# Performance work log

Measured on AMD Instinct MI355X. Metric: run time of the kernel, lower is better.

The kernel has to match this reference:

```python
import jax, jax.numpy as jnp
import numpy as np

S = 3072        # total packed tokens
E = 1280        # d_model
H = 20          # encoder_attention_heads
D = E // H      # head_dim = 64
NSEG = 16       # number of packed audio chunks


def setup_inputs() -> dict:
    key = jax.random.key(0)
    ks = jax.random.split(key, 9)
    w = lambda k, shape: (jax.random.normal(k, shape, jnp.float32) * 0.02)
    hidden_states = jax.random.normal(ks[0], (S, E), jnp.float32)
    cu_seqlens = (jnp.arange(NSEG + 1, dtype=jnp.int32) * (S // NSEG))
    return {
        "hidden_states": hidden_states,
        "Wq": w(ks[1], (E, E)), "bq": w(ks[2], (E,)),
        "Wk": w(ks[3], (E, E)),                      # k_proj has no bias
        "Wv": w(ks[4], (E, E)), "bv": w(ks[5], (E,)),
        "Wo": w(ks[6], (E, E)), "bo": w(ks[7], (E,)),
        "cu_seqlens": cu_seqlens,
    }


def reference(hidden_states, Wq, bq, Wk, Wv, bv, Wo, bo, cu_seqlens):
    Sq, Em = hidden_states.shape
    Dh = Em // H
    # projections (torch Linear: x @ W.T + b)
    q = (hidden_states @ Wq.T + bq).reshape(Sq, H, Dh).transpose(1, 0, 2)  # [H,S,D]
    k = (hidden_states @ Wk.T).reshape(Sq, H, Dh).transpose(1, 0, 2)       # [H,S,D]
    v = (hidden_states @ Wv.T + bv).reshape(Sq, H, Dh).transpose(1, 0, 2)  # [H,S,D]
    # block-diagonal additive mask from cu_seqlens (vectorized equivalent of
    # the original Python loop): tokens attend only within their own segment.
    pos = jnp.arange(Sq)
    seg = jnp.searchsorted(cu_seqlens[1:], pos, side="right")              # segment id per token
    same = seg[:, None] == seg[None, :]                                    # [S,S]
    bias = jnp.where(same, 0.0, jnp.finfo(q.dtype).min)
    attn = jnp.einsum("hqd,hkd->hqk", q, k) / np.sqrt(Dh).astype(q.dtype)  # [H,S,S]
    attn = jax.nn.softmax(attn + bias, axis=-1)
    out = jnp.einsum("hqk,hkd->hqd", attn, v)                              # [H,S,D]
    out = out.transpose(1, 0, 2).reshape(Sq, Em)
    return out @ Wo.T + bo
```

## Files before the change

kernel.cpp:

```cpp
#include <hip/hip_runtime.h>
#include <hip/hip_bf16.h>
#include <stdint.h>

#define S_TOK 3072
#define E_DIM 1280
#define H_NUM 20
#define D_HEAD 64
#define NSEG 16

typedef __attribute__((ext_vector_type(8))) short short8;
typedef __attribute__((ext_vector_type(4))) float f32x4;

__device__ __forceinline__ unsigned short f2bf(float f){
  union { float f; unsigned int i; } u; u.f = f;
  unsigned int r = u.i + 0x7FFFu + ((u.i >> 16) & 1u);
  return (unsigned short)(r >> 16);
}

__device__ __forceinline__ void gload_lds16(const void* g, void* l){
  __builtin_amdgcn_global_load_lds((__attribute__((address_space(1))) void*)(g),
                                   (__attribute__((address_space(3))) void*)(l), 16, 0, 0);
}

__global__ void cvt_all(const float* __restrict__ hs,
                        const float* __restrict__ w0, const float* __restrict__ w1,
                        const float* __restrict__ w2,
                        unsigned short* __restrict__ hsb,
                        unsigned short* __restrict__ dqkv,
                        int nHS4, int nW4){
  int i = blockIdx.x * blockDim.x + threadIdx.x;
  const float* src;
  unsigned short* dst;
  size_t sj, dj;
  if (i < nHS4){
    src = hs; dst = hsb; sj = i; dj = i;
  } else {
    int t = i - nHS4;
    int w = t / nW4;
    if (w >= 3) return;
    int j = t - w * nW4;
    src = (w == 0) ? w0 : (w == 1) ? w1 : w2;
    sj = j;
    dst = dqkv; dj = (size_t)w * nW4 + j;
  }
  float4 v = reinterpret_cast<const float4*>(src)[sj];
  ushort4 o;
  o.x = f2bf(v.x); o.y = f2bf(v.y); o.z = f2bf(v.z); o.w = f2bf(v.w);
  reinterpret_cast<ushort4*>(dst)[dj] = o;
}

template<int MODE>
__global__ __launch_bounds__(MODE==0?512:256, MODE==0?2:2) void gemm_ph(
    const unsigned short* __restrict__ A,
    const unsigned short* __restrict__ Bp,
    const float* __restrict__ bias0,
    const float* __restrict__ bias1,
    unsigned short* __restrict__ Oq,
    unsigned short* __restrict__ Ok,
    unsigned short* __restrict__ Ov,
    float* __restrict__ Of,
    int M, int N, int K)
{
  constexpr int BM    = MODE==0 ? 256 : 128;
  constexpr int BLOCK = MODE==0 ? 512 : 256;
  constexpr int HR    = BM/2;
  constexpr int HS    = HR*64;
  constexpr int MR2   = MODE==0 ? 4 : 2;

  __shared__ __align__(16) unsigned short SH[8*HS];

  const int nwg = gridDim.x;
  const int xcd = blockIdx.x & 7, ix = blockIdx.x >> 3;
  const int qq = nwg >> 3, rr8 = nwg & 7;
  const int wg = (xcd < rr8 ? xcd*(qq+1) : rr8*(qq+1) + (xcd-rr8)*qq) + ix;
  const int nbn = N / BM;
  const int sgn = nbn / 5;
  const int st = wg / 20, ii = wg % 20;
  const int bm = (st / sgn) * 4 + ii / 5;
  const int bn = (st % sgn) * 5 + ii % 5;
  const int row0 = bm * BM, col0 = bn * BM;

  const int tid  = threadIdx.x;
  const int lane = tid & 63;
  const int w    = tid >> 6;
  const int wm   = MODE==0 ? (w >> 2) : (w >> 1);
  const int wn   = MODE==0 ? (w & 3) : (w & 1);

  const f32x4 fz = {0.f, 0.f, 0.f, 0.f};
  f32x4 acc[4][MR2][2];
#pragma unroll
  for (int qd = 0; qd < 4; ++qd)
#pragma unroll
    for (int m = 0; m < MR2; ++m)
#pragma unroll
      for (int n = 0; n < 2; ++n) acc[qd][m][n] = fz;

  const int s1 = tid, s2 = BLOCK + tid;
  const int r1 = s1 >> 3, ks1 = (s1 & 7) ^ (r1 & 7);
  const int r2 = s2 >> 3, ks2 = (s2 & 7) ^ (r2 & 7);

  auto stA = [&](int h, int t){
    unsigned short* d = SH + ((t & 1) * 4 + h) * HS;
    const unsigned short* g = A + (size_t)(row0 + h*HR) * K + (t << 6);
    gload_lds16(g + (size_t)r1*K + ks1*8, d + s1*8);
    gload_lds16(g + (size_t)r2*K + ks2*8, d + s2*8);
  };
  auto stB = [&](int h, int t){
    unsigned short* d = SH + ((t & 1) * 4 + 2 + h) * HS;
    const unsigned short* g = Bp + (size_t)(col0 + h*HR) * K + (t << 6);
    gload_lds16(g + (size_t)r1*K + ks1*8, d + s1*8);
    gload_lds16(g + (size_t)r2*K + ks2*8, d + s2*8);
  };

  short8 af[MR2][2], bf0[2][2], bf1[2][2];
  auto RA = [&](int mh, int db){
    const unsigned short* Ah = SH + (db*4 + mh)*HS;
#pragma unroll
    for (int m = 0; m < MR2; ++m){
      int ra = wm*(HR/2) + m*16 + (lane & 15);
#pragma unroll
      for (int kk = 0; kk < 2; ++kk){
        int sl = kk*4 + (lane >> 4);
        af[m][kk] = *reinterpret_cast<const short8*>(&Ah[ra*64 + ((sl ^ (ra & 7)))*8]);
      }
    }
  };
  auto RB = [&](int nh, int db, short8 (*bf)[2]){
    const unsigned short* Bh = SH + (db*4 + 2 + nh)*HS;
#pragma unroll
    for (int n = 0; n < 2; ++n){
      int rb = wn*32 + n*16 + (lane & 15);
#pragma unroll
      for (int kk = 0; kk < 2; ++kk){
        int sl = kk*4 + (lane >> 4);
        bf[n][kk] = *reinterpret_cast<const short8*>(&Bh[rb*64 + ((sl ^ (rb & 7)))*8]);
      }
    }
  };

#define MF_Q(QD, BF)                                                          \
  do {                                                                        \
    __builtin_amdgcn_s_setprio(1);                                            \
    _Pragma("unroll")                                                         \
    for (int kk = 0; kk < 2; ++kk)                                            \
      _Pragma("unroll")                                                       \
      for (int m = 0; m < MR2; ++m)                                           \
        _Pragma("unroll")                                                     \
        for (int n = 0; n < 2; ++n)                                           \
          acc[QD][m][n] = __builtin_amdgcn_mfma_f32_16x16x32_bf16(            \
              af[m][kk], BF[n][kk], acc[QD][m][n], 0, 0, 0);                  \
    __builtin_amdgcn_s_setprio(0);                                            \
  } while (0)

#define LGKM0 do { asm volatile("s_waitcnt lgkmcnt(0)" ::: "memory");         \
                   __builtin_amdgcn_sched_barrier(0); } while (0)
#define BAR   __builtin_amdgcn_s_barrier()

  const int nk = K >> 6;
  stA(0,0); stB(0,0); stB(1,0); stA(1,0);
  stA(0,1); stB(0,1); stB(1,1);
  asm volatile("s_waitcnt vmcnt(6)" ::: "memory");
  BAR;

  for (int t = 0; t < nk - 1; ++t){
    const int db = t & 1;
    const bool f2 = (t + 2 < nk);
    RA(0, db); RB(0, db, bf0);
    stA(1, t+1);
    BAR; LGKM0; MF_Q(0, bf0); BAR;
    RB(1, db, bf1);
    if (f2) stA(0, t+2);
    BAR; LGKM0; MF_Q(1, bf1); BAR;
    RA(1, db);
    if (f2) stB(0, t+2);
    BAR; LGKM0; MF_Q(2, bf1); BAR;
    if (f2) stB(1, t+2);
    BAR; MF_Q(3, bf0);
    if (f2) asm volatile("s_waitcnt vmcnt(6)" ::: "memory");
    else    asm volatile("s_waitcnt vmcnt(4)" ::: "memory");
    BAR;
  }
  {
    const int db = (nk - 1) & 1;
    RA(0, db); RB(0, db, bf0);
    BAR; LGKM0; MF_Q(0, bf0);
    asm volatile("s_waitcnt vmcnt(2)" ::: "memory");
    BAR;
    RB(1, db, bf1);
    BAR; LGKM0; MF_Q(1, bf1);
    asm volatile("s_waitcnt vmcnt(0)" ::: "memory");
    BAR;
    RA(1, db);
    BAR; LGKM0; MF_Q(2, bf1); BAR;
    MF_Q(3, bf0);
  }
  __syncthreads();

  if (MODE == 0){
    unsigned short* Cs = SH;
    const int CSTR = 264;
    const int mat = col0 / E_DIM;
    const int cc0 = col0 - mat * E_DIM;
    unsigned short* dst = (mat == 0) ? Oq : ((mat == 1) ? Ok : Ov);
    float bb[2][2];
#pragma unroll
    for (int nh = 0; nh < 2; ++nh)
#pragma unroll
      for (int n = 0; n < 2; ++n){
        int cc = cc0 + nh*128 + wn*32 + n*16 + (lane & 15);
        bb[nh][n] = (mat == 0) ? bias0[cc] : (mat == 2 ? bias1[cc] : 0.0f);
      }
#pragma unroll
    for (int ph = 0; ph < 2; ++ph){
#pragma unroll
      for (int q2i = 0; q2i < 2; ++q2i){
        const int qd = ph*2 + q2i;
        const int nh = (qd >> 1) ^ (qd & 1);
#pragma unroll
        for (int m = 0; m < MR2; ++m)
#pragma unroll
          for (int n = 0; n < 2; ++n)
#pragma unroll
            for (int j = 0; j < 4; ++j){
              int rr = wm*64 + m*16 + (lane >> 4)*4 + j;
              int c  = nh*128 + wn*32 + n*16 + (lane & 15);
              Cs[rr * CSTR + c] = f2bf(acc[qd][m][n][j] + bb[nh][n]);
            }
      }
      __syncthreads();
#pragma unroll
      for (int i = 0; i < 8; ++i){
        int tk  = i * 512 + tid;
        int p   = tk >> 10;
        int idx = tk & 1023;
        int rr  = idx >> 3, sq = idx & 7;
        short8 vv = *reinterpret_cast<const short8*>(&Cs[rr * CSTR + p * 64 + sq * 8]);
        int gr = row0 + ph * 128 + rr;
        int hh = (cc0 >> 6) + p;
        *reinterpret_cast<short8*>(&dst[((size_t)hh * S_TOK + gr) * D_HEAD + sq * 8]) = vv;
      }
      __syncthreads();
    }
  } else {
    float bc[2][2];
#pragma unroll
    for (int nh = 0; nh < 2; ++nh)
#pragma unroll
      for (int n = 0; n < 2; ++n)
        bc[nh][n] = bias0[col0 + nh*64 + wn*32 + n*16 + (lane & 15)];
#pragma unroll
    for (int qd = 0; qd < 4; ++qd){
      const int mh = qd >> 1;
      const int nh = (qd >> 1) ^ (qd & 1);
#pragma unroll
      for (int m = 0; m < MR2; ++m)
#pragma unroll
        for (int n = 0; n < 2; ++n){
          int c = col0 + nh*64 + wn*32 + n*16 + (lane & 15);
#pragma unroll
          for (int j = 0; j < 4; ++j){
            int r = row0 + mh*64 + wm*32 + m*16 + (lane >> 4)*4 + j;
            Of[(size_t)r * E_DIM + c] = acc[qd][m][n][j] + bc[nh][n];
          }
        }
    }
  }
#undef MF_Q
#undef LGKM0
#undef BAR
}

#define VSTR 200
#define PSTR 72
#define ATTN_BLKS (H_NUM * NSEG * 3)
__global__ __launch_bounds__(256, 3) void attn_kernel(
    const unsigned short* __restrict__ Q,
    const unsigned short* __restrict__ Kb,
    const unsigned short* __restrict__ V,
    const int* __restrict__ cu,
    unsigned short* __restrict__ O,
    const float* __restrict__ Wo,
    unsigned short* __restrict__ wob,
    int nW4)
{
  __shared__ __align__(16) unsigned short Vt[64*VSTR];
  __shared__ __align__(16) unsigned short Pw[4][16][PSTR];

  const int bid  = blockIdx.x;
  if (bid >= ATTN_BLKS){
    int i = (bid - ATTN_BLKS) * 256 + threadIdx.x;
    if (i < nW4){
      float4 v = reinterpret_cast<const float4*>(Wo)[i];
      ushort4 o;
      o.x = f2bf(v.x); o.y = f2bf(v.y); o.z = f2bf(v.z); o.w = f2bf(v.w);
      reinterpret_cast<ushort4*>(wob)[i] = o;
    }
    return;
  }
  const int unit = bid / 3;
  const int third= bid - unit*3;
  const int h    = unit >> 4;
  const int seg  = unit & 15;
  const int s0   = cu[seg];
  const int L    = cu[seg + 1] - s0;
  if (L <= 0) return;

  const int tid  = threadIdx.x;
  const int lane = tid & 63;
  const int w    = tid >> 6;
  const int row0g = third*64 + w*16;

  const unsigned short* qh = Q  + (size_t)h * S_TOK * D_HEAD;
  const unsigned short* kh = Kb + (size_t)h * S_TOK * D_HEAD;
  const unsigned short* vh = V  + (size_t)h * S_TOK * D_HEAD;

#pragma unroll
  for (int i = 0; i < 6; ++i){
    int task = i*256 + tid;
    int sr   = task % 192;
    int grp  = task / 192;
    int svr  = s0 + (sr < L ? sr : L - 1);
    short8 vv = *reinterpret_cast<const short8*>(vh + (size_t)svr*64 + grp*8);
#pragma unroll
    for (int j = 0; j < 8; ++j) Vt[(grp*8 + j)*VSTR + sr] = (unsigned short)vv[j];
  }

  short8 qf[2];
#pragma unroll
  for (int kk = 0; kk < 2; ++kk){
    int r  = row0g + (lane & 15);
    int sr = s0 + (r < L ? r : L - 1);
    qf[kk] = *reinterpret_cast<const short8*>(qh + (size_t)sr*64 + kk*32 + (lane >> 4)*8);
  }

  __syncthreads();

  const f32x4 fz = {0.f, 0.f, 0.f, 0.f};
  const float SCL = 0.125f * 1.44269504088896f;

  f32x4 sacc[12];
#pragma unroll
  for (int nt = 0; nt < 12; ++nt) sacc[nt] = fz;

#pragma unroll
  for (int nt = 0; nt < 12; ++nt){
    int rb = nt*16 + (lane & 15);
    int sr = s0 + (rb < L ? rb : L - 1);
    const unsigned short* kr = kh + (size_t)sr*64 + (lane >> 4)*8;
    short8 kf0 = *reinterpret_cast<const short8*>(kr);
    short8 kf1 = *reinterpret_cast<const short8*>(kr + 32);
    sacc[nt] = __builtin_amdgcn_mfma_f32_16x16x32_bf16(qf[0], kf0, sacc[nt], 0, 0, 0);
    sacc[nt] = __builtin_amdgcn_mfma_f32_16x16x32_bf16(qf[1], kf1, sacc[nt], 0, 0, 0);
  }

  float rinv[4];
#pragma unroll
  for (int j = 0; j < 4; ++j){
    float mx = -1e30f;
#pragma unroll
    for (int nt = 0; nt < 12; ++nt){
      int c = nt*16 + (lane & 15);
      float vv = (c < L) ? sacc[nt][j] : -1e30f;
      sacc[nt][j] = vv;
      mx = fmaxf(mx, vv);
    }
    mx = fmaxf(mx, __shfl_xor(mx, 1, 64));
    mx = fmaxf(mx, __shfl_xor(mx, 2, 64));
    mx = fmaxf(mx, __shfl_xor(mx, 4, 64));
    mx = fmaxf(mx, __shfl_xor(mx, 8, 64));
    float sum = 0.f;
#pragma unroll
    for (int nt = 0; nt < 12; ++nt){
      float pp = exp2f((sacc[nt][j] - mx) * SCL);
      sacc[nt][j] = pp;
      sum += pp;
    }
    sum += __shfl_xor(sum, 1, 64);
    sum += __shfl_xor(sum, 2, 64);
    sum += __shfl_xor(sum, 4, 64);
    sum += __shfl_xor(sum, 8, 64);
    rinv[j] = 1.0f / sum;
  }

  f32x4 oacc[4];
#pragma unroll
  for (int nt = 0; nt < 4; ++nt) oacc[nt] = fz;

#pragma unroll
  for (int kk = 0; kk < 6; ++kk){
#pragma unroll
    for (int ntl = 0; ntl < 2; ++ntl){
      int nt = kk*2 + ntl;
#pragma unroll
      for (int j = 0; j < 4; ++j)
        Pw[w][(lane >> 4)*4 + j][ntl*16 + (lane & 15)] = f2bf(sacc[nt][j]);
    }
    short8 pf = *reinterpret_cast<const short8*>(&Pw[w][lane & 15][(lane >> 4)*8]);
#pragma unroll
    for (int nt4 = 0; nt4 < 4; ++nt4){
      int dcol = nt4*16 + (lane & 15);
      short8 vf = *reinterpret_cast<const short8*>(&Vt[dcol*VSTR + kk*32 + (lane >> 4)*8]);
      oacc[nt4] = __builtin_amdgcn_mfma_f32_16x16x32_bf16(pf, vf, oacc[nt4], 0, 0, 0);
    }
  }

#pragma unroll
  for (int nt4 = 0; nt4 < 4; ++nt4)
#pragma unroll
    for (int j = 0; j < 4; ++j)
      Pw[w][(lane >> 4)*4 + j][nt4*16 + (lane & 15)] = f2bf(oacc[nt4][j] * rinv[j]);

  {
    int r = lane >> 2;
    int gr = row0g + r;
    if (gr < L){
#pragma unroll
      for (int part = 0; part < 2; ++part){
        int c0 = (lane & 3)*16 + part*8;
        short8 vv = *reinterpret_cast<const short8*>(&Pw[w][r][c0]);
        *reinterpret_cast<short8*>(&O[(size_t)(s0 + gr) * E_DIM + h*64 + c0]) = vv;
      }
    }
  }
}

extern "C" void kernel_launch(void* const* d_in, const int* in_sizes, int n_in,
                              void* d_out, int out_size, void* d_ws, size_t ws_size,
                              hipStream_t stream)
{
  const float* hs = (const float*)d_in[0];
  const float* Wq = (const float*)d_in[1];
  const float* bq = (const float*)d_in[2];
  const float* Wk = (const float*)d_in[3];
  const float* Wv = (const float*)d_in[4];
  const float* bv = (const float*)d_in[5];
  const float* Wo = (const float*)d_in[6];
  const float* bo = (const float*)d_in[7];
  const int*   cu = (const int*)d_in[8];
  float* out = (float*)d_out;

  unsigned short* p = (unsigned short*)d_ws;
  unsigned short* hsb  = p; p += (size_t)S_TOK * E_DIM;
  unsigned short* wqkv = p; p += (size_t)3 * E_DIM * E_DIM;
  unsigned short* wob  = p; p += (size_t)E_DIM * E_DIM;
  unsigned short* qb   = p; p += (size_t)S_TOK * E_DIM;
  unsigned short* kb   = p; p += (size_t)S_TOK * E_DIM;
  unsigned short* vb   = p; p += (size_t)S_TOK * E_DIM;
  unsigned short* aob  = p; p += (size_t)S_TOK * E_DIM;

  const int nHS4 = S_TOK * E_DIM / 4;
  const int nW4  = E_DIM * E_DIM / 4;
  const int nCvt = nHS4 + 3 * nW4;
  cvt_all<<<(nCvt + 255) / 256, 256, 0, stream>>>(hs, Wq, Wk, Wv, hsb, wqkv, nHS4, nW4);

  gemm_ph<0><<<(S_TOK/256) * (3*E_DIM/256), 512, 0, stream>>>(
      hsb, wqkv, bq, bv, qb, kb, vb, nullptr, S_TOK, 3*E_DIM, E_DIM);

  const int cvtWoBlks = (nW4 + 255) / 256;
  attn_kernel<<<ATTN_BLKS + cvtWoBlks, 256, 0, stream>>>(
      qb, kb, vb, cu, aob, Wo, wob, nW4);

  gemm_ph<1><<<(S_TOK/128) * (E_DIM/128), 256, 0, stream>>>(
      aob, wob, bo, nullptr, nullptr, nullptr, nullptr, out, S_TOK, E_DIM, E_DIM);
}
```

Baseline: 95.49 us.

## Retile QKV GEMM to 192x256 blocks and shorten prefetch pipeline

The QKV projection GEMM drops its shared template and uses 192x256 tiles, so the grid goes from 180 to 240 workgroups, which fills the CUs of the 256-CU part better. Its double-buffered pipeline now prefetches one k-step ahead with fewer barriers per iteration instead of two steps ahead. The output GEMM becomes its own kernel with the same restructured one-ahead pipeline. The trade-off is a shallower prefetch, which leaves less room to hide global load latency, plus a more complex tile-index mapping and epilogue.

```diff
diff --git a/kernel.cpp b/kernel.cpp
--- a/kernel.cpp
+++ b/kernel.cpp
@@ -49,8 +49,11 @@
   reinterpret_cast<ushort4*>(dst)[dj] = o;
 }
 
-template<int MODE>
-__global__ __launch_bounds__(MODE==0?512:256, MODE==0?2:2) void gemm_ph(
+#define LGKM0 do { asm volatile("s_waitcnt lgkmcnt(0)" ::: "memory");         \
+                   __builtin_amdgcn_sched_barrier(0); } while (0)
+#define BAR   __builtin_amdgcn_s_barrier()
+
+__global__ __launch_bounds__(512, 2) void gemm_qkv(
     const unsigned short* __restrict__ A,
     const unsigned short* __restrict__ Bp,
     const float* __restrict__ bias0,
@@ -58,82 +61,77 @@
     unsigned short* __restrict__ Oq,
     unsigned short* __restrict__ Ok,
     unsigned short* __restrict__ Ov,
-    float* __restrict__ Of,
-    int M, int N, int K)
+    int K)
 {
-  constexpr int BM    = MODE==0 ? 256 : 128;
-  constexpr int BLOCK = MODE==0 ? 512 : 256;
-  constexpr int HR    = BM/2;
-  constexpr int HS    = HR*64;
-  constexpr int MR2   = MODE==0 ? 4 : 2;
-
-  __shared__ __align__(16) unsigned short SH[8*HS];
+  constexpr int SLOT = (192 + 256) * 64;
+  __shared__ __align__(16) unsigned short SH[2 * SLOT];
 
   const int nwg = gridDim.x;
   const int xcd = blockIdx.x & 7, ix = blockIdx.x >> 3;
-  const int qq = nwg >> 3, rr8 = nwg & 7;
-  const int wg = (xcd < rr8 ? xcd*(qq+1) : rr8*(qq+1) + (xcd-rr8)*qq) + ix;
-  const int nbn = N / BM;
-  const int sgn = nbn / 5;
+  const int wg = xcd * (nwg >> 3) + ix;
   const int st = wg / 20, ii = wg % 20;
-  const int bm = (st / sgn) * 4 + ii / 5;
-  const int bn = (st % sgn) * 5 + ii % 5;
-  const int row0 = bm * BM, col0 = bn * BM;
+  const int bm = (st / 3) * 4 + ii / 5;
+  const int bn = (st % 3) * 5 + ii % 5;
+  const int row0 = bm * 192, col0 = bn * 256;
 
   const int tid  = threadIdx.x;
   const int lane = tid & 63;
   const int w    = tid >> 6;
-  const int wm   = MODE==0 ? (w >> 2) : (w >> 1);
-  const int wn   = MODE==0 ? (w & 3) : (w & 1);
+  const int wm   = w >> 2;
+  const int wn   = w & 3;
 
   const f32x4 fz = {0.f, 0.f, 0.f, 0.f};
-  f32x4 acc[4][MR2][2];
+  f32x4 acc[4][3][2];
 #pragma unroll
   for (int qd = 0; qd < 4; ++qd)
 #pragma unroll
-    for (int m = 0; m < MR2; ++m)
+    for (int m = 0; m < 3; ++m)
 #pragma unroll
       for (int n = 0; n < 2; ++n) acc[qd][m][n] = fz;
 
-  const int s1 = tid, s2 = BLOCK + tid;
-  const int r1 = s1 >> 3, ks1 = (s1 & 7) ^ (r1 & 7);
-  const int r2 = s2 >> 3, ks2 = (s2 & 7) ^ (r2 & 7);
-
-  auto stA = [&](int h, int t){
-    unsigned short* d = SH + ((t & 1) * 4 + h) * HS;
-    const unsigned short* g = A + (size_t)(row0 + h*HR) * K + (t << 6);
-    gload_lds16(g + (size_t)r1*K + ks1*8, d + s1*8);
-    gload_lds16(g + (size_t)r2*K + ks2*8, d + s2*8);
+  auto stA = [&](int t){
+    unsigned short* d = SH + (t & 1) * SLOT;
+    const unsigned short* g = A + (size_t)row0 * K + (t << 6);
+#pragma unroll
+    for (int i = 0; i < 3; ++i){
+      int s = i * 512 + tid;
+      int r = s >> 3, ks = (s & 7) ^ (r & 7);
+      gload_lds16(g + (size_t)r * K + ks * 8, d + s * 8);
+    }
   };
   auto stB = [&](int h, int t){
-    unsigned short* d = SH + ((t & 1) * 4 + 2 + h) * HS;
-    const unsigned short* g = Bp + (size_t)(col0 + h*HR) * K + (t << 6);
-    gload_lds16(g + (size_t)r1*K + ks1*8, d + s1*8);
-    gload_lds16(g + (size_t)r2*K + ks2*8, d + s2*8);
-  };
-
-  short8 af[MR2][2], bf0[2][2], bf1[2][2];
+    unsigned short* d = SH + (t & 1) * SLOT + 12288 + h * 8192;
+    const unsigned short* g = Bp + (size_t)(col0 + h * 128) * K + (t << 6);
+#pragma unroll
+    for (int i = 0; i < 2; ++i){
+      int s = i * 512 + tid;
+      int r = s >> 3, ks = (s & 7) ^ (r & 7);
+      gload_lds16(g + (size_t)r * K + ks * 8, d + s * 8);
+    }
+  };
+
+  short8 af[3][2], bf0[2][2], bf1[2][2];
   auto RA = [&](int mh, int db){
-    const unsigned short* Ah = SH + (db*4 + mh)*HS;
-#pragma unroll
-    for (int m = 0; m < MR2; ++m){
-      int ra = wm*(HR/2) + m*16 + (lane & 15);
+    const unsigned short* Ah = SH + db * SLOT;
+#pragma unroll
+    for (int m = 0; m < 3; ++m){
+      int ra = mh * 96 + wm * 48 + m * 16 + (lane & 15);
 #pragma unroll
       for (int kk = 0; kk < 2; ++kk){
-        int sl = kk*4 + (lane >> 4);
-        af[m][kk] = *reinterpret_cast<const short8*>(&Ah[ra*64 + ((sl ^ (ra & 7)))*8]);
+        int sl = kk * 4 + (lane >> 4);
+        af[m][kk] = *reinterpret_cast<const short8*>(&Ah[ra * 64 + ((sl ^ (ra & 7))) * 8]);
       }
     }
   };
   auto RB = [&](int nh, int db, short8 (*bf)[2]){
-    const unsigned short* Bh = SH + (db*4 + 2 + nh)*HS;
+    const unsigned short* Bb = SH + db * SLOT + 12288;
 #pragma unroll
     for (int n = 0; n < 2; ++n){
-      int rb = wn*32 + n*16 + (lane & 15);
+      int rb = nh * 128 + wn * 32 + n * 16 + (lane & 15);
 #pragma unroll
       for (int kk = 0; kk < 2; ++kk){
-        int sl = kk*4 + (lane >> 4);
-        bf[n][kk] = *reinterpret_cast<const short8*>(&Bh[rb*64 + ((sl ^ (rb & 7)))*8]);
+        int sl = kk * 4 + (lane >> 4);
+        bf[n][kk] = *reinterpret_cast<const short8*>(&Bb[rb * 64 + ((sl ^ (rb & 7))) * 8]);
       }
     }
   };
@@ -144,7 +142,7 @@
     _Pragma("unroll")                                                         \
     for (int kk = 0; kk < 2; ++kk)                                            \
       _Pragma("unroll")                                                       \
-      for (int m = 0; m < MR2; ++m)                                           \
+      for (int m = 0; m < 3; ++m)                                             \
         _Pragma("unroll")                                                     \
         for (int n = 0; n < 2; ++n)                                           \
           acc[QD][m][n] = __builtin_amdgcn_mfma_f32_16x16x32_bf16(            \
@@ -152,51 +150,32 @@
     __builtin_amdgcn_s_setprio(0);                                            \
   } while (0)
 
-#define LGKM0 do { asm volatile("s_waitcnt lgkmcnt(0)" ::: "memory");         \
-                   __builtin_amdgcn_sched_barrier(0); } while (0)
-#define BAR   __builtin_amdgcn_s_barrier()
-
   const int nk = K >> 6;
-  stA(0,0); stB(0,0); stB(1,0); stA(1,0);
-  stA(0,1); stB(0,1); stB(1,1);
-  asm volatile("s_waitcnt vmcnt(6)" ::: "memory");
-  BAR;
-
-  for (int t = 0; t < nk - 1; ++t){
+  stA(0); stB(0, 0); stB(1, 0);
+  for (int t = 0; t < nk; ++t){
     const int db = t & 1;
-    const bool f2 = (t + 2 < nk);
+    const bool nx = (t + 1 < nk);
+    asm volatile("s_waitcnt vmcnt(2)" ::: "memory");
+    BAR;
     RA(0, db); RB(0, db, bf0);
-    stA(1, t+1);
-    BAR; LGKM0; MF_Q(0, bf0); BAR;
+    if (nx) stA(t + 1);
+    LGKM0; MF_Q(0, bf0);
+    if (nx) asm volatile("s_waitcnt vmcnt(3)" ::: "memory");
+    else    asm volatile("s_waitcnt vmcnt(0)" ::: "memory");
+    BAR;
     RB(1, db, bf1);
-    if (f2) stA(0, t+2);
-    BAR; LGKM0; MF_Q(1, bf1); BAR;
+    if (nx) stB(0, t + 1);
+    LGKM0; MF_Q(1, bf1);
+    BAR;
     RA(1, db);
-    if (f2) stB(0, t+2);
-    BAR; LGKM0; MF_Q(2, bf1); BAR;
-    if (f2) stB(1, t+2);
-    BAR; MF_Q(3, bf0);
-    if (f2) asm volatile("s_waitcnt vmcnt(6)" ::: "memory");
-    else    asm volatile("s_waitcnt vmcnt(4)" ::: "memory");
-    BAR;
-  }
+    if (nx) stB(1, t + 1);
+    LGKM0; MF_Q(2, bf1);
+    BAR;
+    MF_Q(3, bf0);
+  }
+  __syncthreads();
+
   {
-    const int db = (nk - 1) & 1;
-    RA(0, db); RB(0, db, bf0);
-    BAR; LGKM0; MF_Q(0, bf0);
-    asm volatile("s_waitcnt vmcnt(2)" ::: "memory");
-    BAR;
-    RB(1, db, bf1);
-    BAR; LGKM0; MF_Q(1, bf1);
-    asm volatile("s_waitcnt vmcnt(0)" ::: "memory");
-    BAR;
-    RA(1, db);
-    BAR; LGKM0; MF_Q(2, bf1); BAR;
-    MF_Q(3, bf0);
-  }
-  __syncthreads();
-
-  if (MODE == 0){
     unsigned short* Cs = SH;
     const int CSTR = 264;
     const int mat = col0 / E_DIM;
@@ -207,67 +186,185 @@
     for (int nh = 0; nh < 2; ++nh)
 #pragma unroll
       for (int n = 0; n < 2; ++n){
-        int cc = cc0 + nh*128 + wn*32 + n*16 + (lane & 15);
+        int cc = cc0 + nh * 128 + wn * 32 + n * 16 + (lane & 15);
         bb[nh][n] = (mat == 0) ? bias0[cc] : (mat == 2 ? bias1[cc] : 0.0f);
       }
 #pragma unroll
     for (int ph = 0; ph < 2; ++ph){
 #pragma unroll
       for (int q2i = 0; q2i < 2; ++q2i){
-        const int qd = ph*2 + q2i;
+        const int qd = ph * 2 + q2i;
         const int nh = (qd >> 1) ^ (qd & 1);
 #pragma unroll
-        for (int m = 0; m < MR2; ++m)
+        for (int m = 0; m < 3; ++m)
 #pragma unroll
           for (int n = 0; n < 2; ++n)
 #pragma unroll
             for (int j = 0; j < 4; ++j){
-              int rr = wm*64 + m*16 + (lane >> 4)*4 + j;
-              int c  = nh*128 + wn*32 + n*16 + (lane & 15);
+              int rr = wm * 48 + m * 16 + (lane >> 4) * 4 + j;
+              int c  = nh * 128 + wn * 32 + n * 16 + (lane & 15);
               Cs[rr * CSTR + c] = f2bf(acc[qd][m][n][j] + bb[nh][n]);
             }
       }
       __syncthreads();
 #pragma unroll
-      for (int i = 0; i < 8; ++i){
+      for (int i = 0; i < 6; ++i){
         int tk  = i * 512 + tid;
-        int p   = tk >> 10;
-        int idx = tk & 1023;
+        int p   = tk / 768;
+        int idx = tk - p * 768;
         int rr  = idx >> 3, sq = idx & 7;
         short8 vv = *reinterpret_cast<const short8*>(&Cs[rr * CSTR + p * 64 + sq * 8]);
-        int gr = row0 + ph * 128 + rr;
+        int gr = row0 + ph * 96 + rr;
         int hh = (cc0 >> 6) + p;
         *reinterpret_cast<short8*>(&dst[((size_t)hh * S_TOK + gr) * D_HEAD + sq * 8]) = vv;
       }
       __syncthreads();
     }
-  } else {
-    float bc[2][2];
-#pragma unroll
-    for (int nh = 0; nh < 2; ++nh)
-#pragma unroll
-      for (int n = 0; n < 2; ++n)
-        bc[nh][n] = bias0[col0 + nh*64 + wn*32 + n*16 + (lane & 15)];
-#pragma unroll
-    for (int qd = 0; qd < 4; ++qd){
-      const int mh = qd >> 1;
-      const int nh = (qd >> 1) ^ (qd & 1);
-#pragma unroll
-      for (int m = 0; m < MR2; ++m)
-#pragma unroll
-        for (int n = 0; n < 2; ++n){
-          int c = col0 + nh*64 + wn*32 + n*16 + (lane & 15);
-#pragma unroll
-          for (int j = 0; j < 4; ++j){
-            int r = row0 + mh*64 + wm*32 + m*16 + (lane >> 4)*4 + j;
-            Of[(size_t)r * E_DIM + c] = acc[qd][m][n][j] + bc[nh][n];
-          }
+  }
+#undef MF_Q
+}
+
+__global__ __launch_bounds__(256, 2) void gemm_out(
+    const unsigned short* __restrict__ A,
+    const unsigned short* __restrict__ Bp,
+    const float* __restrict__ bias0,
+    float* __restrict__ Of,
+    int K)
+{
+  constexpr int HS = 64 * 64;
+  __shared__ __align__(16) unsigned short SH[8 * HS];
+
+  const int nwg = gridDim.x;
+  const int xcd = blockIdx.x & 7, ix = blockIdx.x >> 3;
+  const int wg = xcd * (nwg >> 3) + ix;
+  const int st = wg / 20, ii = wg % 20;
+  const int bm = (st / 2) * 4 + ii / 5;
+  const int bn = (st % 2) * 5 + ii % 5;
+  const int row0 = bm * 128, col0 = bn * 128;
+
+  const int tid  = threadIdx.x;
+  const int lane = tid & 63;
+  const int w    = tid >> 6;
+  const int wm   = w >> 1;
+  const int wn   = w & 1;
+
+  const f32x4 fz = {0.f, 0.f, 0.f, 0.f};
+  f32x4 acc[4][2][2];
+#pragma unroll
+  for (int qd = 0; qd < 4; ++qd)
+#pragma unroll
+    for (int m = 0; m < 2; ++m)
+#pragma unroll
+      for (int n = 0; n < 2; ++n) acc[qd][m][n] = fz;
+
+  const int s1 = tid, s2 = 256 + tid;
+  const int r1 = s1 >> 3, ks1 = (s1 & 7) ^ (r1 & 7);
+  const int r2 = s2 >> 3, ks2 = (s2 & 7) ^ (r2 & 7);
+
+  auto stA = [&](int h, int t){
+    unsigned short* d = SH + ((t & 1) * 4 + h) * HS;
+    const unsigned short* g = A + (size_t)(row0 + h * 64) * K + (t << 6);
+    gload_lds16(g + (size_t)r1 * K + ks1 * 8, d + s1 * 8);
+    gload_lds16(g + (size_t)r2 * K + ks2 * 8, d + s2 * 8);
+  };
+  auto stB = [&](int h, int t){
+    unsigned short* d = SH + ((t & 1) * 4 + 2 + h) * HS;
+    const unsigned short* g = Bp + (size_t)(col0 + h * 64) * K + (t << 6);
+    gload_lds16(g + (size_t)r1 * K + ks1 * 8, d + s1 * 8);
+    gload_lds16(g + (size_t)r2 * K + ks2 * 8, d + s2 * 8);
+  };
+
+  short8 af[2][2], bf0[2][2], bf1[2][2];
+  auto RA = [&](int mh, int db){
+    const unsigned short* Ah = SH + (db * 4 + mh) * HS;
+#pragma unroll
+    for (int m = 0; m < 2; ++m){
+      int ra = wm * 32 + m * 16 + (lane & 15);
+#pragma unroll
+      for (int kk = 0; kk < 2; ++kk){
+        int sl = kk * 4 + (lane >> 4);
+        af[m][kk] = *reinterpret_cast<const short8*>(&Ah[ra * 64 + ((sl ^ (ra & 7))) * 8]);
+      }
+    }
+  };
+  auto RB = [&](int nh, int db, short8 (*bf)[2]){
+    const unsigned short* Bh = SH + (db * 4 + 2 + nh) * HS;
+#pragma unroll
+    for (int n = 0; n < 2; ++n){
+      int rb = wn * 32 + n * 16 + (lane & 15);
+#pragma unroll
+      for (int kk = 0; kk < 2; ++kk){
+        int sl = kk * 4 + (lane >> 4);
+        bf[n][kk] = *reinterpret_cast<const short8*>(&Bh[rb * 64 + ((sl ^ (rb & 7))) * 8]);
+      }
+    }
+  };
+
+#define MF_Q(QD, BF)                                                          \
+  do {                                                                        \
+    __builtin_amdgcn_s_setprio(1);                                            \
+    _Pragma("unroll")                                                         \
+    for (int kk = 0; kk < 2; ++kk)                                            \
+      _Pragma("unroll")                                                       \
+      for (int m = 0; m < 2; ++m)                                             \
+        _Pragma("unroll")                                                     \
+        for (int n = 0; n < 2; ++n)                                           \
+          acc[QD][m][n] = __builtin_amdgcn_mfma_f32_16x16x32_bf16(            \
+              af[m][kk], BF[n][kk], acc[QD][m][n], 0, 0, 0);                  \
+    __builtin_amdgcn_s_setprio(0);                                            \
+  } while (0)
+
+  const int nk = K >> 6;
+  stA(0, 0); stB(0, 0); stB(1, 0); stA(1, 0);
+  for (int t = 0; t < nk; ++t){
+    const int db = t & 1;
+    const bool nx = (t + 1 < nk);
+    asm volatile("s_waitcnt vmcnt(4)" ::: "memory");
+    BAR;
+    RA(0, db); RB(0, db, bf0);
+    if (nx) stA(0, t + 1);
+    LGKM0; MF_Q(0, bf0);
+    if (nx) asm volatile("s_waitcnt vmcnt(4)" ::: "memory");
+    else    asm volatile("s_waitcnt vmcnt(2)" ::: "memory");
+    BAR;
+    RB(1, db, bf1);
+    if (nx) stB(0, t + 1);
+    LGKM0; MF_Q(1, bf1);
+    if (nx) asm volatile("s_waitcnt vmcnt(4)" ::: "memory");
+    else    asm volatile("s_waitcnt vmcnt(0)" ::: "memory");
+    BAR;
+    RA(1, db);
+    if (nx) stB(1, t + 1);
+    LGKM0; MF_Q(2, bf1);
+    BAR;
+    if (nx) stA(1, t + 1);
+    MF_Q(3, bf0);
+  }
+  __syncthreads();
+
+  float bc[2][2];
+#pragma unroll
+  for (int nh = 0; nh < 2; ++nh)
+#pragma unroll
+    for (int n = 0; n < 2; ++n)
+      bc[nh][n] = bias0[col0 + nh * 64 + wn * 32 + n * 16 + (lane & 15)];
+#pragma unroll
+  for (int qd = 0; qd < 4; ++qd){
+    const int mh = qd >> 1;
+    const int nh = (qd >> 1) ^ (qd & 1);
+#pragma unroll
+    for (int m = 0; m < 2; ++m)
+#pragma unroll
+      for (int n = 0; n < 2; ++n){
+        int c = col0 + nh * 64 + wn * 32 + n * 16 + (lane & 15);
+#pragma unroll
+        for (int j = 0; j < 4; ++j){
+          int r = row0 + mh * 64 + wm * 32 + m * 16 + (lane >> 4) * 4 + j;
+          Of[(size_t)r * E_DIM + c] = acc[qd][m][n][j] + bc[nh][n];
         }
-    }
+      }
   }
 #undef MF_Q
-#undef LGKM0
-#undef BAR
 }
 
 #define VSTR 200
@@ -453,13 +550,13 @@
   const int nCvt = nHS4 + 3 * nW4;
   cvt_all<<<(nCvt + 255) / 256, 256, 0, stream>>>(hs, Wq, Wk, Wv, hsb, wqkv, nHS4, nW4);
 
-  gemm_ph<0><<<(S_TOK/256) * (3*E_DIM/256), 512, 0, stream>>>(
-      hsb, wqkv, bq, bv, qb, kb, vb, nullptr, S_TOK, 3*E_DIM, E_DIM);
+  gemm_qkv<<<(S_TOK/192) * (3*E_DIM/256), 512, 0, stream>>>(
+      hsb, wqkv, bq, bv, qb, kb, vb, E_DIM);
 
   const int cvtWoBlks = (nW4 + 255) / 256;
   attn_kernel<<<ATTN_BLKS + cvtWoBlks, 256, 0, stream>>>(
       qb, kb, vb, cu, aob, Wo, wob, nW4);
 
-  gemm_ph<1><<<(S_TOK/128) * (E_DIM/128), 256, 0, stream>>>(
-      aob, wob, bo, nullptr, nullptr, nullptr, nullptr, out, S_TOK, E_DIM, E_DIM);
-}
+  gemm_out<<<(S_TOK/128) * (E_DIM/128), 256, 0, stream>>>(
+      aob, wob, bo, out, E_DIM);
+}
```

Result: faster. 87.19 us (-8.7%).
